# Optimization experiments

Measured on AMD Instinct MI355X. Metric: run time of the kernel, lower is better.

Reference implementation:

```python
import jax, jax.numpy as jnp
import numpy as np

V = 32000   # vocab
E = 512     # hidden_size (d_model)
NH = 8      # num_heads
DH = E // NH
NL = 2      # num_layers
FF = 2048   # TransformerDecoderLayer default dim_feedforward
MAXLEN = 24 # cfg.max_length -> gen_len (no target given)
S, B = 48, 8
TRANS = 14
INIT = TRANS - 2            # tgt = transform[1:-1]
LF = INIT + MAXLEN - 1      # final tgt length after the loop
EPS = 1e-5
NEG = -1e9


def pos_encoding(length, d):
    pos = np.arange(length, dtype=np.float32)[:, None]
    div = np.exp(-np.log(10000.0) * np.arange(0, d, 2, dtype=np.float32) / d)
    pe = np.zeros((length, d), dtype=np.float32)
    pe[:, 0::2] = np.sin(pos * div)
    pe[:, 1::2] = np.cos(pos * div)
    return jnp.asarray(pe)


def setup_inputs() -> dict:
    key = jax.random.key(0)
    ks = jax.random.split(key, 12)
    s = 0.02
    return {
        "enc_outputs": jax.random.normal(ks[0], (S, B, E), jnp.float32),
        "transform": jax.random.randint(ks[1], (TRANS, B), 0, V),
        "tf_ratio": 0,
        "emb_table": jax.random.normal(ks[2], (V, E), jnp.float32) * s,
        "sa_w": jax.random.normal(ks[3], (NL, 3 * E, E), jnp.float32) * s,
        "sa_b": jnp.zeros((NL, 3 * E), jnp.float32),
        "sa_ow": jax.random.normal(ks[4], (NL, E, E), jnp.float32) * s,
        "sa_ob": jnp.zeros((NL, E), jnp.float32),
        "ca_w": jax.random.normal(ks[5], (NL, 3 * E, E), jnp.float32) * s,
        "ca_b": jnp.zeros((NL, 3 * E), jnp.float32),
        "ca_ow": jax.random.normal(ks[6], (NL, E, E), jnp.float32) * s,
        "ca_ob": jnp.zeros((NL, E), jnp.float32),
        "ff1_w": jax.random.normal(ks[7], (NL, FF, E), jnp.float32) * s,
        "ff1_b": jnp.zeros((NL, FF), jnp.float32),
        "ff2_w": jax.random.normal(ks[8], (NL, E, FF), jnp.float32) * s,
        "ff2_b": jnp.zeros((NL, E), jnp.float32),
        "ln_g": jnp.ones((NL, 3, E), jnp.float32),
        "ln_b": jnp.zeros((NL, 3, E), jnp.float32),
        "out_w": jax.random.normal(ks[9], (V, E), jnp.float32) * s,
        "out_b": jnp.zeros((V,), jnp.float32),
    }


def _ln(x, g, b):
    m = jnp.mean(x, -1, keepdims=True)
    v = jnp.mean((x - m) ** 2, -1, keepdims=True)
    return (x - m) * jax.lax.rsqrt(v + EPS) * g + b


def _mha(q_in, kv_in, w, b, ow, ob, mask):
    # q_in [Lq,B,E], kv_in [Lk,B,E]; PyTorch packed in_proj [3E,E]
    wq, wk, wv = jnp.split(w, 3, 0)
    bq, bk, bv = jnp.split(b, 3, 0)
    proj = lambda x, wm, bm: (x @ wm.T + bm).reshape(x.shape[0], x.shape[1], NH, DH)
    q, k, v = proj(q_in, wq, bq), proj(kv_in, wk, bk), proj(kv_in, wv, bv)
    sc = jnp.einsum('qbhd,kbhd->bhqk', q, k) / np.sqrt(DH).astype(np.float32)
    if mask is not None:
        sc = sc + mask
    a = jax.nn.softmax(sc, -1)
    o = jnp.einsum('bhqk,kbhd->qbhd', a, v).reshape(q_in.shape[0], q_in.shape[1], E)
    return o @ ow.T + ob


def _decoder(x, mem, mask, p):
    # post-norm TransformerDecoderLayer: self-attn -> cross-attn -> relu FFN
    for l in range(NL):
        x = _ln(x + _mha(x, x, p['sa_w'][l], p['sa_b'][l], p['sa_ow'][l], p['sa_ob'][l], mask),
                p['ln_g'][l, 0], p['ln_b'][l, 0])
        x = _ln(x + _mha(x, mem, p['ca_w'][l], p['ca_b'][l], p['ca_ow'][l], p['ca_ob'][l], None),
                p['ln_g'][l, 1], p['ln_b'][l, 1])
        h = jax.nn.relu(x @ p['ff1_w'][l].T + p['ff1_b'][l]) @ p['ff2_w'][l].T + p['ff2_b'][l]
        x = _ln(x + h, p['ln_g'][l, 2], p['ln_b'][l, 2])
    return x


def reference(enc_outputs, transform, tf_ratio, emb_table, sa_w, sa_b, sa_ow, sa_ob,
              ca_w, ca_b, ca_ow, ca_ob, ff1_w, ff1_b, ff2_w, ff2_b, ln_g, ln_b,
              out_w, out_b):
    # tf_ratio == 0 -> no teacher forcing; gen_len = max_length (no target attr)
    p = dict(sa_w=sa_w, sa_b=sa_b, sa_ow=sa_ow, sa_ob=sa_ob, ca_w=ca_w, ca_b=ca_b,
             ca_ow=ca_ow, ca_ob=ca_ob, ff1_w=ff1_w, ff1_b=ff1_b, ff2_w=ff2_w,
             ff2_b=ff2_b, ln_g=ln_g, ln_b=ln_b)
    pe = pos_encoding(MAXLEN, E)
    # causal mask over the fixed-size buffer; padded (future) slots cannot
    # influence valid positions, so full-buffer passes == torch prefix passes.
    mask = jnp.where(jnp.tril(jnp.ones((LF, LF), bool)), 0.0, NEG)
    tgt0 = emb_table[transform[1:-1]] + pe[:INIT][:, None, :]   # [INIT,B,E]
    buf = jnp.zeros((LF, B, E), jnp.float32).at[:INIT].set(tgt0)

    def step(buf, i):
        h = _decoder(buf, enc_outputs, mask, p)
        pos = INIT - 1 + i                        # last valid position
        pred = jnp.argmax(h[pos] @ out_w.T + out_b, axis=-1)   # [B]
        # torch re-embeds the single predicted token -> PE position 0
        emb = emb_table[pred] + pe[0]
        return buf.at[pos + 1].set(emb), None

    buf, _ = jax.lax.scan(step, buf, jnp.arange(MAXLEN - 1))
    h = _decoder(buf, enc_outputs, mask, p)       # final loop iteration's pass
    return h @ out_w.T + out_b                    # dec_outputs [LF,B,V]
```

## Files before the change

kernel.cpp:

```cpp
#include <hip/hip_runtime.h>
#include <hip/hip_bf16.h>
#include <math.h>

#define V    32000
#define E    512
#define NH   8
#define DH   64
#define NL   2
#define FF   2048
#define MAXLEN 24
#define S    48
#define B    8
#define TRANS 14
#define INIT 12
#define LF   35

#define NB   256
#define NT   1024

typedef float f4 __attribute__((ext_vector_type(4)));

__device__ inline float wsum(float v) {
#pragma unroll
  for (int off = 32; off; off >>= 1) v += __shfl_xor(v, off);
  return v;
}
__device__ inline float wmax(float v) {
#pragma unroll
  for (int off = 32; off; off >>= 1) v = fmaxf(v, __shfl_xor(v, off));
  return v;
}

__device__ inline float ldc(const float* p) {
  return __hip_atomic_load(p, __ATOMIC_RELAXED, __HIP_MEMORY_SCOPE_AGENT);
}
__device__ inline void stc(float* p, float v) {
  __hip_atomic_store(p, v, __ATOMIC_RELAXED, __HIP_MEMORY_SCOPE_AGENT);
}
__device__ inline float2 ldc8(const float* p) {
  union { unsigned long long u; float2 f; } c;
  c.u = __hip_atomic_load((const unsigned long long*)p, __ATOMIC_RELAXED, __HIP_MEMORY_SCOPE_AGENT);
  return c.f;
}
__device__ inline void stc8(float* p, float x, float y) {
  union { unsigned long long u; float f[2]; } c; c.f[0] = x; c.f[1] = y;
  __hip_atomic_store((unsigned long long*)p, c.u, __ATOMIC_RELAXED, __HIP_MEMORY_SCOPE_AGENT);
}
__device__ inline int ldci(const int* p) {
  return __hip_atomic_load(p, __ATOMIC_RELAXED, __HIP_MEMORY_SCOPE_AGENT);
}
__device__ inline void stci(int* p, int v) {
  __hip_atomic_store(p, v, __ATOMIC_RELAXED, __HIP_MEMORY_SCOPE_AGENT);
}

#define CMB(v, idx, ov, oi) do { if ((ov) > (v) || ((ov) == (v) && (oi) < (idx))) { (v) = (ov); (idx) = (oi); } } while (0)


__global__ void embed_init_k(const int* __restrict__ transform, const float* __restrict__ emb,
                             float* __restrict__ xbuf) {
  int t = blockIdx.x;
  int pos = t >> 3, b = t & 7;
  int tok = transform[(1 + pos) * B + b];
  for (int d = threadIdx.x; d < E; d += blockDim.x) {
    double div = exp(-log(10000.0) * (double)(d & ~1) / (double)E);
    double ang = (double)pos * div;
    float pe = (d & 1) ? (float)cos(ang) : (float)sin(ang);
    xbuf[(size_t)t * E + d] = emb[(size_t)tok * E + d] + pe;
  }
}

template <int K>
__global__ __launch_bounds__(256) void gemm_k(
    const float* __restrict__ x, const float* __restrict__ W, const float* __restrict__ bias,
    int ntok, int nout, int route, int relu,
    float* __restrict__ out0, float* __restrict__ out1, float* __restrict__ out2) {
  constexpr int K4 = K / 4;
  constexpr int J  = K / 256;
  __shared__ float4 xt[8][K4];
  const int tid = threadIdx.x;
  const int lane = tid & 63;
  const int o = blockIdx.x * 4 + (tid >> 6);

  float4 wr[J];
  if (o < nout) {
    const float4* Wr = (const float4*)(W + (size_t)o * K);
#pragma unroll
    for (int j = 0; j < J; ++j) wr[j] = Wr[lane + 64 * j];
  }

  const int ng = ntok >> 3;
  for (int g = 0; g < ng; ++g) {
    if (g) __syncthreads();
    const float4* xg = (const float4*)(x + (size_t)g * 8 * K);
    float4* xf = &xt[0][0];
    for (int i = tid; i < 8 * K4; i += 256) xf[i] = xg[i];
    __syncthreads();
    if (o < nout) {
      float acc[8] = {0, 0, 0, 0, 0, 0, 0, 0};
#pragma unroll
      for (int j = 0; j < J; ++j) {
        float4 w = wr[j];
#pragma unroll
        for (int tt = 0; tt < 8; ++tt) {
          float4 xv = xt[tt][lane + 64 * j];
          acc[tt] += w.x * xv.x + w.y * xv.y + w.z * xv.z + w.w * xv.w;
        }
      }
#pragma unroll
      for (int tt = 0; tt < 8; ++tt) acc[tt] = wsum(acc[tt]);
      if (lane == 0) {
        float bo = bias[o];
#pragma unroll
        for (int tt = 0; tt < 8; ++tt) {
          float v = acc[tt] + bo;
          if (relu) v = fmaxf(v, 0.f);
          int t = g * 8 + tt;
          if (route == 0) {
            out0[(size_t)t * nout + o] = v;
          } else if (route == 1) {
            if (o < E) out0[(size_t)t * E + o] = v;
            else if (o < 2 * E) out1[(size_t)t * E + (o - E)] = v;
            else out2[(size_t)t * E + (o - 2 * E)] = v;
          } else {
            if (o < E) out0[(size_t)t * E + o] = v;
            else out1[(size_t)t * E + (o - E)] = v;
          }
        }
      }
    }
  }
}

__global__ __launch_bounds__(256) void attn_k(
    const float* __restrict__ q, const float* __restrict__ Kc, const float* __restrict__ Vc,
    float* __restrict__ outp, int p0, int nq, int nk_fixed, int causal) {
  const int tid = threadIdx.x;
  const int lane = tid & 63;
  const int u = blockIdx.x * 4 + (tid >> 6);
  if (u >= nq * 64) return;
  const int qi = u >> 6;
  const int r = u & 63;
  const int b = r >> 3, h = r & 7;
  const int nk = causal ? (p0 + qi + 1) : nk_fixed;

  const size_t qoff = (size_t)(qi * B + b) * E + h * DH + lane;
  const float qv = q[qoff];

  float myscore = -INFINITY;
  for (int k = 0; k < nk; ++k) {
    float prod = qv * Kc[(size_t)(k * B + b) * E + h * DH + lane];
    prod = wsum(prod);
    if (lane == k) myscore = prod * 0.125f;
  }
  float m = wmax(myscore);
  float p = (lane < nk) ? expf(myscore - m) : 0.f;
  float denom = wsum(p);
  float a = p / denom;

  float oacc = 0.f;
  for (int k = 0; k < nk; ++k) {
    float ak = __shfl(a, k);
    oacc = fmaf(ak, Vc[(size_t)(k * B + b) * E + h * DH + lane], oacc);
  }
  outp[qoff] = oacc;
}

__global__ __launch_bounds__(256) void add_ln_k(
    const float* __restrict__ xa, const float* __restrict__ xb,
    const float* __restrict__ g, const float* __restrict__ beta,
    float* __restrict__ outp, int ntok) {
  const int tid = threadIdx.x, lane = tid & 63;
  const int t = blockIdx.x * 4 + (tid >> 6);
  if (t >= ntok) return;
  float v[8];
  float s = 0.f;
#pragma unroll
  for (int j = 0; j < 8; ++j) {
    int d = lane + 64 * j;
    v[j] = xa[(size_t)t * E + d] + xb[(size_t)t * E + d];
    s += v[j];
  }
  s = wsum(s);
  float mean = s * (1.f / 512.f);
  float d2 = 0.f;
#pragma unroll
  for (int j = 0; j < 8; ++j) { float dd = v[j] - mean; d2 += dd * dd; }
  d2 = wsum(d2);
  float inv = 1.f / sqrtf(d2 * (1.f / 512.f) + 1e-5f);
#pragma unroll
  for (int j = 0; j < 8; ++j) {
    int d = lane + 64 * j;
    outp[(size_t)t * E + d] = (v[j] - mean) * inv * g[d] + beta[d];
  }
}

#define B_QKV 0
#define B_OW  6144
#define B_CQ  8192
#define B_COW 10240
#define B_FF1 12288
#define B_FF2 20480
#define SW_TOT 28672

__global__ __launch_bounds__(NT, 1) void decode_persist_k(
    const float* __restrict__ emb,
    const float* __restrict__ sa_w, const float* __restrict__ sa_b,
    const float* __restrict__ sa_ow, const float* __restrict__ sa_ob,
    const float* __restrict__ ca_w, const float* __restrict__ ca_b,
    const float* __restrict__ ca_ow, const float* __restrict__ ca_ob,
    const float* __restrict__ ff1_w, const float* __restrict__ ff1_b,
    const float* __restrict__ ff2_w, const float* __restrict__ ff2_b,
    const float* __restrict__ ln_g, const float* __restrict__ ln_b,
    const float* __restrict__ out_w, const float* __restrict__ out_b,
    float* __restrict__ kself, float* __restrict__ vself,
    const float* __restrict__ kcross, const float* __restrict__ vcross,
    float* __restrict__ qbuf, float* __restrict__ attbuf, float* __restrict__ rawbuf,
    float* __restrict__ hbuf, float* __restrict__ amaxbuf,
    float* __restrict__ outp, int* __restrict__ bar) {
  __shared__ __align__(16) float s_w[SW_TOT];
  __shared__ __align__(16) float s_x[8 * E];
  __shared__ __align__(16) float s_raw[8 * E];
  __shared__ __align__(16) float s_q2[64];
  __shared__ __align__(16) float s_attw[64];
  __shared__ __align__(16) float s_part[4][64];
  __shared__ int   s_tok[8];
  __shared__ float s_pv[16][8];
  __shared__ int   s_pi[16][8];

  const int tid  = threadIdx.x;
  const int lane = tid & 63;
  const int wv   = tid >> 6;
  const int bid  = blockIdx.x;
  int gen = 0;

  auto gbar = [&]() {
    ++gen;
    __syncthreads();
    if (tid == 0) stci(&bar[bid * 32], gen);
    if (wv == 0) {
      for (;;) {
        int c0 = ldci(&bar[lane * 32]);
        int c1 = ldci(&bar[(lane + 64) * 32]);
        int c2 = ldci(&bar[(lane + 128) * 32]);
        int c3 = ldci(&bar[(lane + 192) * 32]);
        if (__all(c0 >= gen && c1 >= gen && c2 >= gen && c3 >= gen)) break;
        __builtin_amdgcn_s_sleep(1);
      }
    }
    __syncthreads();
  };

  auto stage_raw = [&](const float* src) {
    for (int k = tid; k < 2048; k += NT) {
      float2 vv = ldc8(src + 2 * k);
      s_raw[2 * k] = vv.x; s_raw[2 * k + 1] = vv.y;
    }
    __syncthreads();
  };
  auto lnstage = [&](int lnidx) {
    if (wv < 8) {
      const float* gg = ln_g + (size_t)lnidx * E;
      const float* be = ln_b + (size_t)lnidx * E;
      float v[8]; float sum = 0.f;
#pragma unroll
      for (int j = 0; j < 8; ++j) {
        int d = lane + 64 * j;
        v[j] = s_x[wv * E + d] + s_raw[wv * E + d];
        sum += v[j];
      }
      sum = wsum(sum);
      float mean = sum * (1.f / 512.f);
      float d2 = 0.f;
#pragma unroll
      for (int j = 0; j < 8; ++j) { float dd = v[j] - mean; d2 += dd * dd; }
      d2 = wsum(d2);
      float inv = 1.f / sqrtf(d2 * (1.f / 512.f) + 1e-5f);
#pragma unroll
      for (int j = 0; j < 8; ++j) {
        int d = lane + 64 * j;
        s_x[wv * E + d] = (v[j] - mean) * inv * gg[d] + be[d];
      }
    }
    __syncthreads();
  };
  auto proj16 = [&](int wbase, const float* srcLDS, const float* biasp, float* dst) {
    int j = wv & 1, b = wv >> 1;
    int r = bid * 2 + j;
    const f4* wp = (const f4*)&s_w[wbase + j * 512];
    f4 w0 = wp[lane], w1 = wp[lane + 64];
    const f4* x4 = (const f4*)(srcLDS + b * E);
    f4 a = w0 * x4[lane] + w1 * x4[lane + 64];
    float acc = a.x + a.y + a.z + a.w;
    acc = wsum(acc);
    if (lane == 0) stc(&dst[b * E + r], acc + biasp[r]);
  };
  auto attn_stage = [&](const float* Kbase, const float* Vbase, int nk) {
    const int b = bid >> 3, h = bid & 7;
    if (wv == 0) {
      s_q2[lane] = ldc(&qbuf[b * E + h * DH + lane]);
      float sc = -INFINITY;
      if (lane < nk) {
        const f4* Kr = (const f4*)(Kbase + ((size_t)lane * B + b) * E + h * DH);
        const f4* Qp = (const f4*)s_q2;
        float a0 = 0.f;
#pragma unroll
        for (int u = 0; u < 16; ++u) {
          f4 kv = Kr[u], qq = Qp[u];
          a0 += kv.x * qq.x + kv.y * qq.y + kv.z * qq.z + kv.w * qq.w;
        }
        sc = a0 * 0.125f;
      }
      float m = wmax(sc);
      float e = (lane < nk) ? expf(sc - m) : 0.f;
      float den = wsum(e);
      s_attw[lane] = e / den;
    }
    __syncthreads();
    if (wv < 4) {
      float o = 0.f;
      for (int k = wv; k < nk; k += 4)
        o = fmaf(s_attw[k], Vbase[((size_t)k * B + b) * E + h * DH + lane], o);
      s_part[wv][lane] = o;
    }
    __syncthreads();
    if (wv == 0)
      stc(&attbuf[b * E + h * DH + lane],
          s_part[0][lane] + s_part[1][lane] + s_part[2][lane] + s_part[3][lane]);
  };

  {
    auto cprow = [&](const float* src, int dstf) {
      f4* d = (f4*)&s_w[dstf]; const f4* s = (const f4*)src;
      for (int k = tid; k < 128; k += NT) d[k] = s[k];
    };
    for (int l = 0; l < NL; ++l) {
      for (int j = 0; j < 6; ++j)
        cprow(sa_w + ((size_t)l * 1536 + bid * 6 + j) * E, B_QKV + (l * 6 + j) * 512);
      for (int j = 0; j < 2; ++j) {
        cprow(sa_ow + ((size_t)l * 512 + bid * 2 + j) * E, B_OW + (l * 2 + j) * 512);
        cprow(ca_w + ((size_t)l * 1536 + bid * 2 + j) * E, B_CQ + (l * 2 + j) * 512);
        cprow(ca_ow + ((size_t)l * 512 + bid * 2 + j) * E, B_COW + (l * 2 + j) * 512);
      }
      for (int j = 0; j < 8; ++j)
        cprow(ff1_w + ((size_t)l * FF + bid * 8 + j) * E, B_FF1 + (l * 8 + j) * 512);
    }
    const int lf2 = bid >> 7;
    for (int j = 0; j < 4; ++j) {
      f4* d = (f4*)&s_w[B_FF2 + j * 2048];
      const f4* s = (const f4*)(ff2_w + ((size_t)lf2 * 512 + (bid & 127) * 4 + j) * FF);
      for (int k = tid; k < 512; k += NT) d[k] = s[k];
    }
    __syncthreads();
  }

  for (int i = 0; i < MAXLEN - 1; ++i) {
    const int p = INIT + i;

    {
      int bw = wv & 7;
      float v = -INFINITY; int ix = 0x7fffffff;
      if (i == 0) {
        const float* row = outp + ((size_t)(INIT - 1) * B + bw) * V;
        for (int jj = lane; jj < V / 2; jj += 64) {
          float2 t = ldc8(row + 2 * jj);
          CMB(v, ix, t.x, 2 * jj);
          CMB(v, ix, t.y, 2 * jj + 1);
        }
      } else {
#pragma unroll
        for (int t = 0; t < 4; ++t) {
          int e = lane * 4 + t;
          float2 pr = ldc8(&amaxbuf[(size_t)(e * 8 + bw) * 2]);
          CMB(v, ix, pr.x, (int)pr.y);
        }
      }
#pragma unroll
      for (int off = 1; off < 64; off <<= 1) {
        float ov = __shfl_xor(v, off); int oi = __shfl_xor(ix, off);
        CMB(v, ix, ov, oi);
      }
      if (lane == 0 && wv < 8) s_tok[bw] = ix;
      __syncthreads();
      int b = tid >> 7, d0 = (tid & 127) * 4;
      int tok = s_tok[b];
      float4 ev = *(const float4*)(emb + (size_t)tok * E + d0);
      s_x[b * E + d0]     = ev.x;
      s_x[b * E + d0 + 1] = ev.y + 1.0f;
      s_x[b * E + d0 + 2] = ev.z;
      s_x[b * E + d0 + 3] = ev.w + 1.0f;
      __syncthreads();
    }

    for (int l = 0; l < NL; ++l) {
      if (wv < 12) {
        int j = wv >> 1, bg = (wv & 1) * 4;
        int r = bid * 6 + j, sec = r >> 9, off = r & 511;
        const f4* wp = (const f4*)&s_w[B_QKV + (l * 6 + j) * 512];
        f4 w0 = wp[lane], w1 = wp[lane + 64];
        float bias = sa_b[(size_t)l * 1536 + r];
        for (int b = bg; b < bg + 4; ++b) {
          const f4* x4 = (const f4*)&s_x[b * E];
          f4 a = w0 * x4[lane] + w1 * x4[lane + 64];
          float acc = a.x + a.y + a.z + a.w;
          acc = wsum(acc);
          if (lane == 0) {
            acc += bias;
            if (sec == 0) stc(&qbuf[b * E + off], acc);
            else if (sec == 1) stc(&kself[((size_t)(l * LF + p) * B + b) * E + off], acc);
            else stc(&vself[((size_t)(l * LF + p) * B + b) * E + off], acc);
          }
        }
      }
      gbar();
      if (bid < 64) attn_stage(kself + (size_t)l * LF * B * E, vself + (size_t)l * LF * B * E, p + 1);
      gbar();
      stage_raw(attbuf);
      proj16(B_OW + l * 1024, s_raw, sa_ob + (size_t)l * E, rawbuf);
      gbar();
      stage_raw(rawbuf);
      lnstage(l * 3 + 0);
      proj16(B_CQ + l * 1024, s_x, ca_b + (size_t)l * 3 * E, qbuf);
      gbar();
      if (bid < 64) attn_stage(kcross + (size_t)l * S * B * E, vcross + (size_t)l * S * B * E, S);
      gbar();
      stage_raw(attbuf);
      proj16(B_COW + l * 1024, s_raw, ca_ob + (size_t)l * E, rawbuf);
      gbar();
      stage_raw(rawbuf);
      lnstage(l * 3 + 1);
      {
        int j = wv >> 1, bg = (wv & 1) * 4;
        int r = bid * 8 + j;
        const f4* wp = (const f4*)&s_w[B_FF1 + (l * 8 + j) * 512];
        f4 w0 = wp[lane], w1 = wp[lane + 64];
        float bias = ff1_b[(size_t)l * FF + r];
        for (int b = bg; b < bg + 4; ++b) {
          const f4* x4 = (const f4*)&s_x[b * E];
          f4 a = w0 * x4[lane] + w1 * x4[lane + 64];
          float acc = a.x + a.y + a.z + a.w;
          acc = wsum(acc);
          if (lane == 0) stc(&hbuf[b * FF + r], fmaxf(acc + bias, 0.f));
        }
      }
      gbar();
      if ((bid >> 7) == l) {
        int b = wv >> 1, j0 = (wv & 1) * 2;
        int r0 = (bid & 127) * 4;
        f4 hv[8];
#pragma unroll
        for (int j = 0; j < 8; ++j) {
          const float* hp = hbuf + b * FF + (j * 64 + lane) * 4;
          float2 a = ldc8(hp), c = ldc8(hp + 2);
          hv[j].x = a.x; hv[j].y = a.y; hv[j].z = c.x; hv[j].w = c.y;
        }
#pragma unroll
        for (int jr = 0; jr < 2; ++jr) {
          int rl = j0 + jr;
          const f4* wp = (const f4*)&s_w[B_FF2 + rl * 2048];
          float acc = 0.f;
#pragma unroll
          for (int j = 0; j < 8; ++j) {
            f4 w = wp[j * 64 + lane];
            acc += w.x * hv[j].x + w.y * hv[j].y + w.z * hv[j].z + w.w * hv[j].w;
          }
          acc = wsum(acc);
          if (lane == 0)
            stc(&rawbuf[b * E + r0 + rl], acc + ff2_b[(size_t)l * 512 + r0 + rl]);
        }
      }
      gbar();
      stage_raw(rawbuf);
      lnstage(l * 3 + 2);
    }

    {
      const int grp = lane >> 3, sub = lane & 7;
      const int idx = wv * 8 + grp;
      const bool valid = idx < 125;
      const int r = bid * 125 + idx;
      float acc[8] = {0, 0, 0, 0, 0, 0, 0, 0};
      if (valid) {
        const f4* wrow = (const f4*)(out_w + (size_t)r * E);
#pragma unroll
        for (int half = 0; half < 2; ++half) {
          f4 w8[8];
#pragma unroll
          for (int j = 0; j < 8; ++j) w8[j] = wrow[(half * 8 + j) * 8 + sub];
#pragma unroll
          for (int b = 0; b < 8; ++b) {
            const f4* x4 = (const f4*)&s_x[b * E];
            float a = 0.f;
#pragma unroll
            for (int j = 0; j < 8; ++j) {
              f4 xx = x4[(half * 8 + j) * 8 + sub];
              a += w8[j].x * xx.x + w8[j].y * xx.y + w8[j].z * xx.z + w8[j].w * xx.w;
            }
            acc[b] += a;
          }
        }
#pragma unroll
        for (int b = 0; b < 8; ++b) {
          acc[b] += __shfl_xor(acc[b], 1);
          acc[b] += __shfl_xor(acc[b], 2);
          acc[b] += __shfl_xor(acc[b], 4);
        }
        if (sub == 0) {
          float bo = out_b[r];
#pragma unroll
          for (int b = 0; b < 8; ++b) {
            acc[b] += bo;
            stc(&outp[((size_t)p * B + b) * V + r], acc[b]);
          }
        }
      }
#pragma unroll
      for (int b = 0; b < 8; ++b) {
        float v = (valid && sub == 0) ? acc[b] : -INFINITY;
        int ix = (valid && sub == 0) ? r : 0x7fffffff;
#pragma unroll
        for (int off = 1; off < 64; off <<= 1) {
          float ov = __shfl_xor(v, off); int oi = __shfl_xor(ix, off);
          CMB(v, ix, ov, oi);
        }
        if (lane == 0) { s_pv[wv][b] = v; s_pi[wv][b] = ix; }
      }
      __syncthreads();
      if (wv == 0) {
        int b = lane & 7, w2 = lane >> 3;
        float v = s_pv[w2][b]; int ix = s_pi[w2][b];
        float v2 = s_pv[w2 + 8][b]; int ix2 = s_pi[w2 + 8][b];
        CMB(v, ix, v2, ix2);
#pragma unroll
        for (int off = 8; off < 64; off <<= 1) {
          float ov = __shfl_xor(v, off); int oi = __shfl_xor(ix, off);
          CMB(v, ix, ov, oi);
        }
        if (lane < 8) stc8(&amaxbuf[(size_t)(bid * 8 + lane) * 2], v, (float)ix);
      }
    }
    gbar();
  }
}

extern "C" void kernel_launch(void* const* d_in, const int* in_sizes, int n_in,
                              void* d_out, int out_size, void* d_ws, size_t ws_size,
                              hipStream_t stream) {
  const float* enc       = (const float*)d_in[0];
  const int*   transform = (const int*)d_in[1];
  const float* emb       = (const float*)d_in[3];
  const float* sa_w  = (const float*)d_in[4];
  const float* sa_b  = (const float*)d_in[5];
  const float* sa_ow = (const float*)d_in[6];
  const float* sa_ob = (const float*)d_in[7];
  const float* ca_w  = (const float*)d_in[8];
  const float* ca_b  = (const float*)d_in[9];
  const float* ca_ow = (const float*)d_in[10];
  const float* ca_ob = (const float*)d_in[11];
  const float* ff1_w = (const float*)d_in[12];
  const float* ff1_b = (const float*)d_in[13];
  const float* ff2_w = (const float*)d_in[14];
  const float* ff2_b = (const float*)d_in[15];
  const float* ln_g  = (const float*)d_in[16];
  const float* ln_b  = (const float*)d_in[17];
  const float* out_w = (const float*)d_in[18];
  const float* out_b = (const float*)d_in[19];
  float* out = (float*)d_out;

  const size_t SELF_SZ  = (size_t)LF * B * E;
  const size_t CROSS_SZ = (size_t)S * B * E;
  float* ws     = (float*)d_ws;
  float* xbuf   = ws;
  float* kself  = xbuf + (size_t)INIT * B * E;
  float* vself  = kself + NL * SELF_SZ;
  float* kcross = vself + NL * SELF_SZ;
  float* vcross = kcross + NL * CROSS_SZ;
  float* qbuf   = vcross + NL * CROSS_SZ;
  float* attbuf = qbuf + 8 * E;
  float* rawbuf = attbuf + 8 * E;
  float* hbuf   = rawbuf + 8 * E;
  float* amaxb  = hbuf + 8 * FF;
  int*   bar    = (int*)(amaxb + 256 * 8 * 2);
  float* act1   = (float*)(bar + 256 * 32);
  float* act2   = act1 + 96 * E;
  float* act3   = act2 + 96 * E;
  float* ffb    = act3 + 96 * E;

  hipMemsetAsync(bar, 0, 256 * 32 * 4, stream);

  embed_init_k<<<INIT * B, 128, 0, stream>>>(transform, emb, xbuf);

  for (int l = 0; l < NL; ++l) {
    gemm_k<E><<<(2 * E) / 4, 256, 0, stream>>>(
        enc, ca_w + ((size_t)l * 3 * E + E) * E, ca_b + (size_t)l * 3 * E + E,
        S * B, 2 * E, 2, 0, kcross + l * CROSS_SZ, vcross + l * CROSS_SZ, nullptr);
  }

  {
    const int p0 = 0, nq = INIT, ntok = nq * B;
    const float* xin = xbuf;
    for (int l = 0; l < NL; ++l) {
      const float* x = (l == 0) ? xin : act1;
      gemm_k<E><<<(3 * E) / 4, 256, 0, stream>>>(
          x, sa_w + (size_t)l * 3 * E * E, sa_b + (size_t)l * 3 * E, ntok, 3 * E, 1, 0,
          act2, kself + l * SELF_SZ, vself + l * SELF_SZ);
      attn_k<<<nq * 16, 256, 0, stream>>>(act2, kself + l * SELF_SZ, vself + l * SELF_SZ,
                                          act3, p0, nq, 0, 1);
      gemm_k<E><<<E / 4, 256, 0, stream>>>(
          act3, sa_ow + (size_t)l * E * E, sa_ob + (size_t)l * E, ntok, E, 0, 0, act2, nullptr, nullptr);
      add_ln_k<<<(ntok + 3) / 4, 256, 0, stream>>>(
          x, act2, ln_g + (size_t)l * 3 * E, ln_b + (size_t)l * 3 * E, act1, ntok);
      gemm_k<E><<<E / 4, 256, 0, stream>>>(
          act1, ca_w + (size_t)l * 3 * E * E, ca_b + (size_t)l * 3 * E, ntok, E, 0, 0, act2, nullptr, nullptr);
      attn_k<<<nq * 16, 256, 0, stream>>>(act2, kcross + l * CROSS_SZ, vcross + l * CROSS_SZ,
                                          act3, p0, nq, S, 0);
      gemm_k<E><<<E / 4, 256, 0, stream>>>(
          act3, ca_ow + (size_t)l * E * E, ca_ob + (size_t)l * E, ntok, E, 0, 0, act2, nullptr, nullptr);
      add_ln_k<<<(ntok + 3) / 4, 256, 0, stream>>>(
          act1, act2, ln_g + (size_t)l * 3 * E + E, ln_b + (size_t)l * 3 * E + E, act1, ntok);
      gemm_k<E><<<FF / 4, 256, 0, stream>>>(
          act1, ff1_w + (size_t)l * FF * E, ff1_b + (size_t)l * FF, ntok, FF, 0, 1, ffb, nullptr, nullptr);
      gemm_k<FF><<<E / 4, 256, 0, stream>>>(
          ffb, ff2_w + (size_t)l * E * FF, ff2_b + (size_t)l * E, ntok, E, 0, 0, act2, nullptr, nullptr);
      add_ln_k<<<(ntok + 3) / 4, 256, 0, stream>>>(
          act1, act2, ln_g + (size_t)l * 3 * E + 2 * E, ln_b + (size_t)l * 3 * E + 2 * E, act1, ntok);
    }
    gemm_k<E><<<V / 4, 256, 0, stream>>>(
        act1, out_w, out_b, ntok, V, 0, 0, out, nullptr, nullptr);
  }

  decode_persist_k<<<NB, NT, 0, stream>>>(
      emb, sa_w, sa_b, sa_ow, sa_ob, ca_w, ca_b, ca_ow, ca_ob,
      ff1_w, ff1_b, ff2_w, ff2_b, ln_g, ln_b, out_w, out_b,
      kself, vself, kcross, vcross,
      qbuf, attbuf, rawbuf, hbuf, amaxb, out, bar);
}
```

Baseline: 5.474 ms.

## Use hierarchical counter grid barrier and write-once arena buffers with plain loads

Replaces the all-to-all flag barrier with a two-level scheme: blocks atomically increment one of 32 counters, block 0 waits for the totals and publishes a single generation flag that every block polls. Per-step scratch buffers (q, attention, residual, FFN hidden, argmax partials) now live in a write-once arena indexed by step, layer and stage. Because no address is ever rewritten, consumers can use ordinary vectorised loads instead of relaxed atomic loads. This trades one extra hop per barrier and a larger workspace for far less barrier polling traffic and cheaper, cacheable reads, but it relies on freshly written addresses never being served stale from a per-CU cache.

```diff
diff --git a/kernel.cpp b/kernel.cpp
--- a/kernel.cpp
+++ b/kernel.cpp
@@ -31,16 +31,8 @@
   return v;
 }
 
-__device__ inline float ldc(const float* p) {
-  return __hip_atomic_load(p, __ATOMIC_RELAXED, __HIP_MEMORY_SCOPE_AGENT);
-}
 __device__ inline void stc(float* p, float v) {
   __hip_atomic_store(p, v, __ATOMIC_RELAXED, __HIP_MEMORY_SCOPE_AGENT);
-}
-__device__ inline float2 ldc8(const float* p) {
-  union { unsigned long long u; float2 f; } c;
-  c.u = __hip_atomic_load((const unsigned long long*)p, __ATOMIC_RELAXED, __HIP_MEMORY_SCOPE_AGENT);
-  return c.f;
 }
 __device__ inline void stc8(float* p, float x, float y) {
   union { unsigned long long u; float f[2]; } c; c.f[0] = x; c.f[1] = y;
@@ -201,6 +193,7 @@
 #define B_FF1 12288
 #define B_FF2 20480
 #define SW_TOT 28672
+#define SLOTS_PER_STEP 23
 
 __global__ __launch_bounds__(NT, 1) void decode_persist_k(
     const float* __restrict__ emb,
@@ -214,9 +207,7 @@
     const float* __restrict__ out_w, const float* __restrict__ out_b,
     float* __restrict__ kself, float* __restrict__ vself,
     const float* __restrict__ kcross, const float* __restrict__ vcross,
-    float* __restrict__ qbuf, float* __restrict__ attbuf, float* __restrict__ rawbuf,
-    float* __restrict__ hbuf, float* __restrict__ amaxbuf,
-    float* __restrict__ outp, int* __restrict__ bar) {
+    float* __restrict__ arena, float* __restrict__ outp, int* __restrict__ bar) {
   __shared__ __align__(16) float s_w[SW_TOT];
   __shared__ __align__(16) float s_x[8 * E];
   __shared__ __align__(16) float s_raw[8 * E];
@@ -233,28 +224,34 @@
   const int bid  = blockIdx.x;
   int gen = 0;
 
+  auto slot = [&](int st, int s) -> float* {
+    return arena + ((size_t)st * SLOTS_PER_STEP + s) * 4096;
+  };
+
   auto gbar = [&]() {
     ++gen;
     __syncthreads();
-    if (tid == 0) stci(&bar[bid * 32], gen);
+    if (tid == 0)
+      __hip_atomic_fetch_add(&bar[(bid & 31) * 32], 1, __ATOMIC_RELAXED, __HIP_MEMORY_SCOPE_AGENT);
+    if (bid == 0 && wv == 0) {
+      const int tgt = gen * 8;
+      for (;;) {
+        int c = (lane < 32) ? ldci(&bar[lane * 32]) : tgt;
+        if (__all(c >= tgt)) break;
+        __builtin_amdgcn_s_sleep(1);
+      }
+      if (lane == 0) stci(&bar[40 * 32], gen);
+    }
     if (wv == 0) {
-      for (;;) {
-        int c0 = ldci(&bar[lane * 32]);
-        int c1 = ldci(&bar[(lane + 64) * 32]);
-        int c2 = ldci(&bar[(lane + 128) * 32]);
-        int c3 = ldci(&bar[(lane + 192) * 32]);
-        if (__all(c0 >= gen && c1 >= gen && c2 >= gen && c3 >= gen)) break;
-        __builtin_amdgcn_s_sleep(1);
-      }
+      while (ldci(&bar[40 * 32]) < gen) __builtin_amdgcn_s_sleep(2);
     }
     __syncthreads();
   };
 
   auto stage_raw = [&](const float* src) {
-    for (int k = tid; k < 2048; k += NT) {
-      float2 vv = ldc8(src + 2 * k);
-      s_raw[2 * k] = vv.x; s_raw[2 * k + 1] = vv.y;
-    }
+    const float4* s4 = (const float4*)src;
+    float4* d4 = (float4*)s_raw;
+    for (int k = tid; k < 1024; k += NT) d4[k] = s4[k];
     __syncthreads();
   };
   auto lnstage = [&](int lnidx) {
@@ -294,10 +291,11 @@
     acc = wsum(acc);
     if (lane == 0) stc(&dst[b * E + r], acc + biasp[r]);
   };
-  auto attn_stage = [&](const float* Kbase, const float* Vbase, int nk) {
+  auto attn_stage = [&](const float* qsrc, const float* Kbase, const float* Vbase,
+                        int nk, float* attdst) {
     const int b = bid >> 3, h = bid & 7;
     if (wv == 0) {
-      s_q2[lane] = ldc(&qbuf[b * E + h * DH + lane]);
+      s_q2[lane] = qsrc[b * E + h * DH + lane];
       float sc = -INFINITY;
       if (lane < nk) {
         const f4* Kr = (const f4*)(Kbase + ((size_t)lane * B + b) * E + h * DH);
@@ -324,7 +322,7 @@
     }
     __syncthreads();
     if (wv == 0)
-      stc(&attbuf[b * E + h * DH + lane],
+      stc(&attdst[b * E + h * DH + lane],
           s_part[0][lane] + s_part[1][lane] + s_part[2][lane] + s_part[3][lane]);
   };
 
@@ -355,22 +353,24 @@
 
   for (int i = 0; i < MAXLEN - 1; ++i) {
     const int p = INIT + i;
+    float* amax_o = slot(i, 0);
 
     {
       int bw = wv & 7;
       float v = -INFINITY; int ix = 0x7fffffff;
       if (i == 0) {
-        const float* row = outp + ((size_t)(INIT - 1) * B + bw) * V;
+        const float2* row = (const float2*)(outp + ((size_t)(INIT - 1) * B + bw) * V);
         for (int jj = lane; jj < V / 2; jj += 64) {
-          float2 t = ldc8(row + 2 * jj);
+          float2 t = row[jj];
           CMB(v, ix, t.x, 2 * jj);
           CMB(v, ix, t.y, 2 * jj + 1);
         }
       } else {
+        const float2* ap = (const float2*)slot(i - 1, 0);
 #pragma unroll
         for (int t = 0; t < 4; ++t) {
           int e = lane * 4 + t;
-          float2 pr = ldc8(&amaxbuf[(size_t)(e * 8 + bw) * 2]);
+          float2 pr = ap[e * 8 + bw];
           CMB(v, ix, pr.x, (int)pr.y);
         }
       }
@@ -392,6 +392,16 @@
     }
 
     for (int l = 0; l < NL; ++l) {
+      float* Lb    = slot(i, 1 + l * 11);
+      float* q_s   = Lb;
+      float* att_s = Lb + 4096;
+      float* raw_s = Lb + 8192;
+      float* q_c   = Lb + 12288;
+      float* att_c = Lb + 16384;
+      float* raw_c = Lb + 20480;
+      float* hb    = Lb + 24576;
+      float* yb    = Lb + 40960;
+
       if (wv < 12) {
         int j = wv >> 1, bg = (wv & 1) * 4;
         int r = bid * 6 + j, sec = r >> 9, off = r & 511;
@@ -405,28 +415,32 @@
           acc = wsum(acc);
           if (lane == 0) {
             acc += bias;
-            if (sec == 0) stc(&qbuf[b * E + off], acc);
+            if (sec == 0) stc(&q_s[b * E + off], acc);
             else if (sec == 1) stc(&kself[((size_t)(l * LF + p) * B + b) * E + off], acc);
             else stc(&vself[((size_t)(l * LF + p) * B + b) * E + off], acc);
           }
         }
       }
       gbar();
-      if (bid < 64) attn_stage(kself + (size_t)l * LF * B * E, vself + (size_t)l * LF * B * E, p + 1);
-      gbar();
-      stage_raw(attbuf);
-      proj16(B_OW + l * 1024, s_raw, sa_ob + (size_t)l * E, rawbuf);
-      gbar();
-      stage_raw(rawbuf);
+      if (bid < 64)
+        attn_stage(q_s, kself + (size_t)l * LF * B * E, vself + (size_t)l * LF * B * E,
+                   p + 1, att_s);
+      gbar();
+      stage_raw(att_s);
+      proj16(B_OW + l * 1024, s_raw, sa_ob + (size_t)l * E, raw_s);
+      gbar();
+      stage_raw(raw_s);
       lnstage(l * 3 + 0);
-      proj16(B_CQ + l * 1024, s_x, ca_b + (size_t)l * 3 * E, qbuf);
-      gbar();
-      if (bid < 64) attn_stage(kcross + (size_t)l * S * B * E, vcross + (size_t)l * S * B * E, S);
-      gbar();
-      stage_raw(attbuf);
-      proj16(B_COW + l * 1024, s_raw, ca_ob + (size_t)l * E, rawbuf);
-      gbar();
-      stage_raw(rawbuf);
+      proj16(B_CQ + l * 1024, s_x, ca_b + (size_t)l * 3 * E, q_c);
+      gbar();
+      if (bid < 64)
+        attn_stage(q_c, kcross + (size_t)l * S * B * E, vcross + (size_t)l * S * B * E,
+                   S, att_c);
+      gbar();
+      stage_raw(att_c);
+      proj16(B_COW + l * 1024, s_raw, ca_ob + (size_t)l * E, raw_c);
+      gbar();
+      stage_raw(raw_c);
       lnstage(l * 3 + 1);
       {
         int j = wv >> 1, bg = (wv & 1) * 4;
@@ -439,20 +453,17 @@
           f4 a = w0 * x4[lane] + w1 * x4[lane + 64];
           float acc = a.x + a.y + a.z + a.w;
           acc = wsum(acc);
-          if (lane == 0) stc(&hbuf[b * FF + r], fmaxf(acc + bias, 0.f));
+          if (lane == 0) stc(&hb[b * FF + r], fmaxf(acc + bias, 0.f));
         }
       }
       gbar();
       if ((bid >> 7) == l) {
         int b = wv >> 1, j0 = (wv & 1) * 2;
         int r0 = (bid & 127) * 4;
+        const f4* h4 = (const f4*)(hb + b * FF);
         f4 hv[8];
 #pragma unroll
-        for (int j = 0; j < 8; ++j) {
-          const float* hp = hbuf + b * FF + (j * 64 + lane) * 4;
-          float2 a = ldc8(hp), c = ldc8(hp + 2);
-          hv[j].x = a.x; hv[j].y = a.y; hv[j].z = c.x; hv[j].w = c.y;
-        }
+        for (int j = 0; j < 8; ++j) hv[j] = h4[j * 64 + lane];
 #pragma unroll
         for (int jr = 0; jr < 2; ++jr) {
           int rl = j0 + jr;
@@ -465,11 +476,11 @@
           }
           acc = wsum(acc);
           if (lane == 0)
-            stc(&rawbuf[b * E + r0 + rl], acc + ff2_b[(size_t)l * 512 + r0 + rl]);
-        }
-      }
-      gbar();
-      stage_raw(rawbuf);
+            stc(&yb[b * E + r0 + rl], acc + ff2_b[(size_t)l * 512 + r0 + rl]);
+        }
+      }
+      gbar();
+      stage_raw(yb);
       lnstage(l * 3 + 2);
     }
 
@@ -509,7 +520,7 @@
 #pragma unroll
           for (int b = 0; b < 8; ++b) {
             acc[b] += bo;
-            stc(&outp[((size_t)p * B + b) * V + r], acc[b]);
+            outp[((size_t)p * B + b) * V + r] = acc[b];
           }
         }
       }
@@ -535,7 +546,7 @@
           float ov = __shfl_xor(v, off); int oi = __shfl_xor(ix, off);
           CMB(v, ix, ov, oi);
         }
-        if (lane < 8) stc8(&amaxbuf[(size_t)(bid * 8 + lane) * 2], v, (float)ix);
+        if (lane < 8) stc8(&amax_o[(size_t)(bid * 8 + lane) * 2], v, (float)ix);
       }
     }
     gbar();
@@ -568,24 +579,21 @@
 
   const size_t SELF_SZ  = (size_t)LF * B * E;
   const size_t CROSS_SZ = (size_t)S * B * E;
+  const size_t ARENA_SZ = (size_t)(MAXLEN - 1) * SLOTS_PER_STEP * 4096;
   float* ws     = (float*)d_ws;
   float* xbuf   = ws;
   float* kself  = xbuf + (size_t)INIT * B * E;
   float* vself  = kself + NL * SELF_SZ;
   float* kcross = vself + NL * SELF_SZ;
   float* vcross = kcross + NL * CROSS_SZ;
-  float* qbuf   = vcross + NL * CROSS_SZ;
-  float* attbuf = qbuf + 8 * E;
-  float* rawbuf = attbuf + 8 * E;
-  float* hbuf   = rawbuf + 8 * E;
-  float* amaxb  = hbuf + 8 * FF;
-  int*   bar    = (int*)(amaxb + 256 * 8 * 2);
-  float* act1   = (float*)(bar + 256 * 32);
+  float* arena  = vcross + NL * CROSS_SZ;
+  int*   bar    = (int*)(arena + ARENA_SZ);
+  float* act1   = (float*)(bar + 64 * 32);
   float* act2   = act1 + 96 * E;
   float* act3   = act2 + 96 * E;
   float* ffb    = act3 + 96 * E;
 
-  hipMemsetAsync(bar, 0, 256 * 32 * 4, stream);
+  hipMemsetAsync(bar, 0, 64 * 32 * 4, stream);
 
   embed_init_k<<<INIT * B, 128, 0, stream>>>(transform, emb, xbuf);
 
@@ -631,6 +639,5 @@
   decode_persist_k<<<NB, NT, 0, stream>>>(
       emb, sa_w, sa_b, sa_ow, sa_ob, ca_w, ca_b, ca_ow, ca_ob,
       ff1_w, ff1_b, ff2_w, ff2_b, ln_g, ln_b, out_w, out_b,
-      kself, vself, kcross, vcross,
-      qbuf, attbuf, rawbuf, hbuf, amaxb, out, bar);
-}
+      kself, vself, kcross, vcross, arena, out, bar);
+}
```

Result: faster. 4.996 ms (-8.7%).
